# Kernel tuning notes

Measured on AMD Instinct MI355X. Metric: run time of the kernel, lower is better.

## Reference

```python
import jax, jax.numpy as jnp
import numpy as np

N = 16384      # n_nodes (ppr is [N, N])
D_IN = 128     # node feature dim
D_H = 64       # encoder output dim
B = 4096       # minibatch of seed nodes
TOPK = 128     # per-row top-k threshold applied to ppr


def _make_topk_ppr(rng, n, topk):
    # Random nonnegative dense PPR surrogate, then zero all but top-k per row,
    # mimicking the topk-thresholded dense buffer in DenseNibblePPR.
    ppr = rng.random((n, n), dtype=np.float32)
    kth = np.partition(ppr, n - topk, axis=1)[:, n - topk : n - topk + 1]
    ppr[ppr < kth] = 0.0
    # normalize rows like a probability diffusion
    ppr /= ppr.sum(axis=1, keepdims=True)
    return ppr


def setup_inputs() -> dict:
    key = jax.random.key(0)
    kx, kw, ki = jax.random.split(key, 3)
    X = jax.random.normal(kx, (N, D_IN), dtype=jnp.float32)
    W = jax.random.normal(kw, (D_IN, D_H), dtype=jnp.float32) * (1.0 / np.sqrt(D_IN))
    b = jnp.zeros((D_H,), dtype=jnp.float32)
    ppr = jnp.asarray(_make_topk_ppr(np.random.default_rng(0), N, TOPK))
    idx = jax.random.randint(ki, (B,), 0, N, dtype=jnp.int64)
    return {"X": X, "ppr": ppr, "W": W, "b": b, "idx": idx}


def reference(X, ppr, W, b, idx):
    # encoder(X): linear encoder over all node features  -> [N, D_H]
    enc = X @ W + b
    # gather PPR diffusion rows for the seed minibatch    -> [B, N]
    rows = jnp.take(ppr, idx, axis=0)
    # dense diffusion GEMM                                -> [B, D_H]
    return rows @ enc
```

## Files before the change

kernel.cpp:

```cpp
#include <hip/hip_runtime.h>
#include <hip/hip_bf16.h>

#define N_NODES 16384
#define D_IN    128
#define D_H     64
#define BATCH   4096
#define CAP     2048

__global__ __launch_bounds__(256) void encoder_kernel(
    const float* __restrict__ X, const float* __restrict__ W,
    const float* __restrict__ b, float* __restrict__ enc)
{
    __shared__ float Xs[4][D_IN];

    const int i0 = blockIdx.x * 4;
    if (threadIdx.x < 128) {
        ((float4*)&Xs[0][0])[threadIdx.x] =
            ((const float4*)(X + (size_t)i0 * D_IN))[threadIdx.x];
    }
    __syncthreads();

    const int r = threadIdx.x >> 6;
    const int h = threadIdx.x & 63;

    float acc = b[h];
    #pragma unroll
    for (int d = 0; d < D_IN; ++d) {
        acc = fmaf(Xs[r][d], W[d * D_H + h], acc);
    }
    enc[(size_t)(i0 + r) * D_H + h] = acc;
}

__global__ __launch_bounds__(256) void diffuse_kernel(
    const float* __restrict__ ppr, const int* __restrict__ idx,
    const float* __restrict__ enc, float* __restrict__ out)
{
    __shared__ int   s_count;
    __shared__ int   s_cols[CAP];
    __shared__ float s_vals[CAP];
    __shared__ float s_acc[4][D_H];

    const int brow = blockIdx.x;
    const int row  = idx[brow];

    if (threadIdx.x == 0) s_count = 0;
    __syncthreads();

    const float4* prow = (const float4*)(ppr + (size_t)row * N_NODES);
    #pragma unroll
    for (int it = 0; it < 16; ++it) {
        const int j = it * 256 + threadIdx.x;
        float4 v = prow[j];
        const int base = j * 4;
        if (v.x != 0.0f) { int p = atomicAdd(&s_count, 1); if (p < CAP) { s_cols[p] = base + 0; s_vals[p] = v.x; } }
        if (v.y != 0.0f) { int p = atomicAdd(&s_count, 1); if (p < CAP) { s_cols[p] = base + 1; s_vals[p] = v.y; } }
        if (v.z != 0.0f) { int p = atomicAdd(&s_count, 1); if (p < CAP) { s_cols[p] = base + 2; s_vals[p] = v.z; } }
        if (v.w != 0.0f) { int p = atomicAdd(&s_count, 1); if (p < CAP) { s_cols[p] = base + 3; s_vals[p] = v.w; } }
    }
    __syncthreads();

    const int K = min(s_count, CAP);
    const int g = threadIdx.x >> 6;
    const int h = threadIdx.x & 63;

    float acc = 0.0f;
    for (int k = g; k < K; k += 4) {
        acc = fmaf(s_vals[k], enc[(size_t)s_cols[k] * D_H + h], acc);
    }
    s_acc[g][h] = acc;
    __syncthreads();

    if (g == 0) {
        float r = s_acc[0][h] + s_acc[1][h] + s_acc[2][h] + s_acc[3][h];
        out[(size_t)brow * D_H + h] = r;
    }
}

extern "C" void kernel_launch(void* const* d_in, const int* in_sizes, int n_in,
                              void* d_out, int out_size, void* d_ws, size_t ws_size,
                              hipStream_t stream) {
    const float* X   = (const float*)d_in[0];
    const float* ppr = (const float*)d_in[1];
    const float* W   = (const float*)d_in[2];
    const float* b   = (const float*)d_in[3];
    const int*   idx = (const int*)d_in[4];
    float* out = (float*)d_out;

    float* enc = (float*)d_ws;

    encoder_kernel<<<N_NODES / 4, 256, 0, stream>>>(X, W, b, enc);
    diffuse_kernel<<<BATCH, 256, 0, stream>>>(ppr, idx, enc, out);
}
```

Baseline: 1.215 ms.

## Batch nontemporal PPR row loads, pack nonzeros, unroll gather, widen encoder blocks

The diffusion kernel now issues eight nontemporal 16-byte loads per thread before compacting nonzeros, which raises memory-level parallelism on the dense row scan. Column and value are packed into one int2 in shared memory, and the capacity is halved to 1024. The gather loop is unrolled by two to overlap the enc loads. The encoder now has each thread compute two rows so each W load is reused, and the grid is halved. The smaller cap still covers the 128 nonzeros per row. Nontemporal loads could hurt if the gathered rows repeat.

```diff
diff --git a/kernel.cpp b/kernel.cpp
--- a/kernel.cpp
+++ b/kernel.cpp
@@ -5,30 +5,34 @@
 #define D_IN    128
 #define D_H     64
 #define BATCH   4096
-#define CAP     2048
+#define CAP     1024
+
+typedef float fvec4 __attribute__((ext_vector_type(4)));
 
 __global__ __launch_bounds__(256) void encoder_kernel(
     const float* __restrict__ X, const float* __restrict__ W,
     const float* __restrict__ b, float* __restrict__ enc)
 {
-    __shared__ float Xs[4][D_IN];
+    __shared__ float Xs[8][D_IN];
 
-    const int i0 = blockIdx.x * 4;
-    if (threadIdx.x < 128) {
-        ((float4*)&Xs[0][0])[threadIdx.x] =
-            ((const float4*)(X + (size_t)i0 * D_IN))[threadIdx.x];
-    }
+    const int i0 = blockIdx.x * 8;
+    ((float4*)&Xs[0][0])[threadIdx.x] =
+        ((const float4*)(X + (size_t)i0 * D_IN))[threadIdx.x];
     __syncthreads();
 
-    const int r = threadIdx.x >> 6;
-    const int h = threadIdx.x & 63;
+    const int rp = threadIdx.x >> 6;
+    const int h  = threadIdx.x & 63;
 
-    float acc = b[h];
+    float acc0 = b[h];
+    float acc1 = acc0;
     #pragma unroll
     for (int d = 0; d < D_IN; ++d) {
-        acc = fmaf(Xs[r][d], W[d * D_H + h], acc);
+        const float wv = W[d * D_H + h];
+        acc0 = fmaf(Xs[2 * rp][d],     wv, acc0);
+        acc1 = fmaf(Xs[2 * rp + 1][d], wv, acc1);
     }
-    enc[(size_t)(i0 + r) * D_H + h] = acc;
+    enc[(size_t)(i0 + 2 * rp)     * D_H + h] = acc0;
+    enc[(size_t)(i0 + 2 * rp + 1) * D_H + h] = acc1;
 }
 
 __global__ __launch_bounds__(256) void diffuse_kernel(
@@ -36,8 +40,7 @@
     const float* __restrict__ enc, float* __restrict__ out)
 {
     __shared__ int   s_count;
-    __shared__ int   s_cols[CAP];
-    __shared__ float s_vals[CAP];
+    __shared__ int2  s_nz[CAP];
     __shared__ float s_acc[4][D_H];
 
     const int brow = blockIdx.x;
@@ -46,16 +49,23 @@
     if (threadIdx.x == 0) s_count = 0;
     __syncthreads();
 
-    const float4* prow = (const float4*)(ppr + (size_t)row * N_NODES);
+    const fvec4* prow = (const fvec4*)(ppr + (size_t)row * N_NODES);
+
     #pragma unroll
-    for (int it = 0; it < 16; ++it) {
-        const int j = it * 256 + threadIdx.x;
-        float4 v = prow[j];
-        const int base = j * 4;
-        if (v.x != 0.0f) { int p = atomicAdd(&s_count, 1); if (p < CAP) { s_cols[p] = base + 0; s_vals[p] = v.x; } }
-        if (v.y != 0.0f) { int p = atomicAdd(&s_count, 1); if (p < CAP) { s_cols[p] = base + 1; s_vals[p] = v.y; } }
-        if (v.z != 0.0f) { int p = atomicAdd(&s_count, 1); if (p < CAP) { s_cols[p] = base + 2; s_vals[p] = v.z; } }
-        if (v.w != 0.0f) { int p = atomicAdd(&s_count, 1); if (p < CAP) { s_cols[p] = base + 3; s_vals[p] = v.w; } }
+    for (int half = 0; half < 2; ++half) {
+        fvec4 v[8];
+        #pragma unroll
+        for (int it = 0; it < 8; ++it)
+            v[it] = __builtin_nontemporal_load(&prow[half * 2048 + it * 256 + threadIdx.x]);
+        #pragma unroll
+        for (int it = 0; it < 8; ++it) {
+            const int base = (half * 2048 + it * 256 + threadIdx.x) * 4;
+            const fvec4 w = v[it];
+            if (w.x != 0.0f) { int p = atomicAdd(&s_count, 1); if (p < CAP) s_nz[p] = make_int2(base + 0, __float_as_int(w.x)); }
+            if (w.y != 0.0f) { int p = atomicAdd(&s_count, 1); if (p < CAP) s_nz[p] = make_int2(base + 1, __float_as_int(w.y)); }
+            if (w.z != 0.0f) { int p = atomicAdd(&s_count, 1); if (p < CAP) s_nz[p] = make_int2(base + 2, __float_as_int(w.z)); }
+            if (w.w != 0.0f) { int p = atomicAdd(&s_count, 1); if (p < CAP) s_nz[p] = make_int2(base + 3, __float_as_int(w.w)); }
+        }
     }
     __syncthreads();
 
@@ -64,15 +74,25 @@
     const int h = threadIdx.x & 63;
 
     float acc = 0.0f;
-    for (int k = g; k < K; k += 4) {
-        acc = fmaf(s_vals[k], enc[(size_t)s_cols[k] * D_H + h], acc);
+    int k = g;
+    for (; k + 4 < K; k += 8) {
+        const int2 a = s_nz[k];
+        const int2 c = s_nz[k + 4];
+        const float ea = enc[(size_t)a.x * D_H + h];
+        const float ec = enc[(size_t)c.x * D_H + h];
+        acc = fmaf(__int_as_float(a.y), ea, acc);
+        acc = fmaf(__int_as_float(c.y), ec, acc);
+    }
+    for (; k < K; k += 4) {
+        const int2 a = s_nz[k];
+        acc = fmaf(__int_as_float(a.y), enc[(size_t)a.x * D_H + h], acc);
     }
     s_acc[g][h] = acc;
     __syncthreads();
 
     if (g == 0) {
-        float r = s_acc[0][h] + s_acc[1][h] + s_acc[2][h] + s_acc[3][h];
-        out[(size_t)brow * D_H + h] = r;
+        out[(size_t)brow * D_H + h] =
+            s_acc[0][h] + s_acc[1][h] + s_acc[2][h] + s_acc[3][h];
     }
 }
 
@@ -88,6 +108,6 @@
 
     float* enc = (float*)d_ws;
 
-    encoder_kernel<<<N_NODES / 4, 256, 0, stream>>>(X, W, b, enc);
+    encoder_kernel<<<N_NODES / 8, 256, 0, stream>>>(X, W, b, enc);
     diffuse_kernel<<<BATCH, 256, 0, stream>>>(ppr, idx, enc, out);
 }
```

Result: faster. 1.189 ms (-2.1%).
